# Performance work log

Measured on AMD Instinct MI355X. Metric: run time of the kernel, lower is better.

The kernel has to match this reference:

```python
import jax, jax.numpy as jnp
import numpy as np

ENC_H = 512
DEC_H = 1024

def setup_inputs() -> dict:
    key = jax.random.key(0)
    k1, k2, k3, k4 = jax.random.split(key, 4)
    B, S = 32, 2048
    s = jax.random.normal(k1, (B, DEC_H), dtype=jnp.float32)
    encoder_outputs = jax.random.normal(k2, (B, S, 2 * ENC_H), dtype=jnp.float32)
    # nn.Linear weights: attn: [dec_h, 2*enc_h + dec_h], v: [1, dec_h]
    fan_in_attn = 2 * ENC_H + DEC_H
    attn_w = jax.random.uniform(k3, (DEC_H, fan_in_attn), dtype=jnp.float32,
                                minval=-1.0, maxval=1.0) / np.sqrt(fan_in_attn)
    v_w = jax.random.uniform(k4, (1, DEC_H), dtype=jnp.float32,
                             minval=-1.0, maxval=1.0) / np.sqrt(DEC_H)
    return {"s": s, "encoder_outputs": encoder_outputs, "attn_w": attn_w, "v_w": v_w}

def reference(s, encoder_outputs, attn_w, v_w):
    # Split attn weight to avoid materializing the repeated/concatenated tensor:
    # cat([s_rep, enc], -1) @ W^T == s @ Ws^T (broadcast over S) + enc @ We^T
    W_s = attn_w[:, :DEC_H]            # [dec_h, dec_h] acts on s
    W_e = attn_w[:, DEC_H:]            # [dec_h, 2*enc_h] acts on encoder_outputs
    proj_s = jnp.einsum('bd,hd->bh', s, W_s)                   # [B, dec_h]
    proj_e = jnp.einsum('bse,he->bsh', encoder_outputs, W_e)   # [B, S, dec_h]
    energy = jnp.tanh(proj_s[:, None, :] + proj_e)             # [B, S, dec_h]
    scores = jnp.einsum('bsh,oh->bs', energy, v_w)             # [B, S]
    return jax.nn.softmax(scores, axis=1)
```

## Files before the change

kernel.cpp:

```cpp
#include <hip/hip_runtime.h>
#include <hip/hip_bf16.h>

#define KDIM 1024
#define HDIM 1024
#define BM   64

typedef __attribute__((ext_vector_type(8))) short bf16x8_t;
typedef __attribute__((ext_vector_type(16))) float f32x16_t;
typedef __attribute__((ext_vector_type(4))) float f32x4_t;
typedef __attribute__((ext_vector_type(4))) unsigned int u32x4_t;
typedef __attribute__((ext_vector_type(2))) unsigned int u32x2_t;

__device__ __forceinline__ unsigned int pack2bf(float a, float b) {
    union { float f; unsigned int u; } ua, ub;
    ua.f = a; ub.f = b;
    unsigned int ra = (ua.u + 0x7fffu + ((ua.u >> 16) & 1u)) >> 16;
    unsigned int rb = (ub.u + 0x7fffu + ((ub.u >> 16) & 1u)) >> 16;
    return ra | (rb << 16);
}

__global__ void cvt_we_k(const float* __restrict__ attn_w, unsigned short* __restrict__ we_t) {
    const int h = blockIdx.x;
    const int t = threadIdx.x;
    const f32x4_t v = *(const f32x4_t*)(attn_w + (size_t)h * 2048 + 1024 + (size_t)t * 4);
    u32x2_t o;
    o[0] = pack2bf(v[0], v[1]);
    o[1] = pack2bf(v[2], v[3]);
    const int ks  = t >> 2;
    const int e15 = (t & 3) * 4;
    *(u32x2_t*)&we_t[(size_t)ks * 16384 + h * 16 + e15] = o;
}

__global__ void proj_s_k(const float* __restrict__ s, const float* __restrict__ attn_w,
                         float* __restrict__ ps) {
    const int h = (blockIdx.x * blockDim.x + threadIdx.x) >> 6;
    const int lane = threadIdx.x & 63;
    const float* wr = attn_w + (size_t)h * 2048;
    float w[16];
#pragma unroll
    for (int i = 0; i < 16; ++i) w[i] = wr[lane + 64 * i];
    for (int b = 0; b < 32; ++b) {
        const float* sr = s + (size_t)b * 1024;
        float a = 0.f;
#pragma unroll
        for (int i = 0; i < 16; ++i) a = fmaf(w[i], sr[lane + 64 * i], a);
#pragma unroll
        for (int off = 32; off >= 1; off >>= 1) a += __shfl_xor(a, off, 64);
        if (lane == 0) ps[b * 1024 + h] = a;
    }
}

__launch_bounds__(512, 2)
__global__ void fused_main_k(const float* __restrict__ enc,
                             const unsigned short* __restrict__ we_t,
                             const float* __restrict__ ps,
                             const float* __restrict__ vw,
                             float* __restrict__ scores) {
    __shared__ unsigned short lds_a[4 * 64 * 128];

    const int t = threadIdx.x;
    const int m_base = blockIdx.x * BM;
    const int bidx = blockIdx.x >> 5;

    const int lane = t & 63;
    const int wid  = t >> 6;
    const int l31  = lane & 31;
    const int h5   = lane >> 5;
    const int hb   = wid * 128;

    const int srow = t >> 4;
    const int sc8  = t & 15;

    auto stage_load = [&](int kc, f32x4_t* r) {
#pragma unroll
        for (int i = 0; i < 2; ++i) {
            const int row = i * 32 + srow;
            const float* p = enc + (size_t)(m_base + row) * KDIM + kc * 128 + sc8 * 8;
            r[2 * i]     = __builtin_nontemporal_load((const f32x4_t*)p);
            r[2 * i + 1] = __builtin_nontemporal_load((const f32x4_t*)(p + 4));
        }
    };
    auto stage_write = [&](int kc, const f32x4_t* r) {
        const int slot = kc & 3;
#pragma unroll
        for (int i = 0; i < 2; ++i) {
            const int row = i * 32 + srow;
            u32x4_t p;
            p[0] = pack2bf(r[2 * i][0], r[2 * i][1]);
            p[1] = pack2bf(r[2 * i][2], r[2 * i][3]);
            p[2] = pack2bf(r[2 * i + 1][0], r[2 * i + 1][1]);
            p[3] = pack2bf(r[2 * i + 1][2], r[2 * i + 1][3]);
            *(u32x4_t*)&lds_a[slot * 8192 + row * 128 + ((sc8 ^ (row & 7)) << 3)] = p;
        }
    };

    const unsigned short* btile = we_t + (size_t)(hb + l31) * 16 + h5 * 8;

    f32x16_t acc[2][4];
#pragma unroll
    for (int m = 0; m < 2; ++m)
#pragma unroll
        for (int nf = 0; nf < 4; ++nf)
#pragma unroll
            for (int r = 0; r < 16; ++r) acc[m][nf][r] = 0.f;

    {
        f32x4_t r0[4], r1[4];
        stage_load(0, r0);
        stage_load(1, r1);
        stage_write(0, r0);
        stage_write(1, r1);
    }
    __syncthreads();

    const int xr = h5 ^ (l31 & 7);
    const int a0base = l31 * 128;
    const int a1base = (32 + l31) * 128;

    for (int kc = 0; kc < 8; ++kc) {
        f32x4_t rs[4];
        if (kc < 6) stage_load(kc + 2, rs);

        const unsigned short* slotp = lds_a + (kc & 3) * 8192;
        const unsigned short* bk = btile + (size_t)(kc * 8) * 16384;
#pragma unroll
        for (int ksl = 0; ksl < 8; ++ksl) {
            const int coff = ((ksl * 2) ^ xr) << 3;
            const bf16x8_t a0 = *(const bf16x8_t*)&slotp[a0base + coff];
            const bf16x8_t a1 = *(const bf16x8_t*)&slotp[a1base + coff];
            const unsigned short* bp = bk + (size_t)ksl * 16384;
            bf16x8_t bfr[4];
#pragma unroll
            for (int nf = 0; nf < 4; ++nf)
                bfr[nf] = *(const bf16x8_t*)(bp + nf * 512);
#pragma unroll
            for (int nf = 0; nf < 4; ++nf) {
                acc[0][nf] = __builtin_amdgcn_mfma_f32_32x32x16_bf16(a0, bfr[nf], acc[0][nf], 0, 0, 0);
                acc[1][nf] = __builtin_amdgcn_mfma_f32_32x32x16_bf16(a1, bfr[nf], acc[1][nf], 0, 0, 0);
            }
        }
        if (kc < 6) stage_write(kc + 2, rs);
        __syncthreads();
    }

    float sc2[2][16];
#pragma unroll
    for (int m = 0; m < 2; ++m)
#pragma unroll
        for (int r = 0; r < 16; ++r) sc2[m][r] = 0.f;

#pragma unroll
    for (int nf = 0; nf < 4; ++nf) {
        const int h = hb + nf * 32 + l31;
        const float pv = ps[bidx * 1024 + h];
        const float vv = vw[h];
#pragma unroll
        for (int m = 0; m < 2; ++m)
#pragma unroll
            for (int r = 0; r < 16; ++r) {
                const float x = acc[m][nf][r] + pv;
                const float e = __expf(2.0f * x);
                const float th = 1.0f - __fdividef(2.0f, e + 1.0f);
                sc2[m][r] = fmaf(vv, th, sc2[m][r]);
            }
    }

#pragma unroll
    for (int off = 1; off < 32; off <<= 1)
#pragma unroll
        for (int m = 0; m < 2; ++m)
#pragma unroll
            for (int r = 0; r < 16; ++r)
                sc2[m][r] += __shfl_xor(sc2[m][r], off, 64);

    __syncthreads();
    float* slds = (float*)lds_a;
    if (l31 == 0) {
#pragma unroll
        for (int m = 0; m < 2; ++m)
#pragma unroll
            for (int r = 0; r < 16; ++r) {
                const int row = m * 32 + (r & 3) + 8 * (r >> 2) + 4 * h5;
                slds[wid * 64 + row] = sc2[m][r];
            }
    }
    __syncthreads();
    if (t < 64) {
        float v = 0.f;
#pragma unroll
        for (int w = 0; w < 8; ++w) v += slds[w * 64 + t];
        scores[m_base + t] = v;
    }
}

__global__ void softmax_k(const float* __restrict__ sc, float* __restrict__ out) {
    const int b = blockIdx.x;
    const int t = threadIdx.x;
    const int lane = t & 63;
    const int w = t >> 6;
    const float* row = sc + (size_t)b * 2048;
    float x[8];
#pragma unroll
    for (int i = 0; i < 8; ++i) x[i] = row[i * 256 + t];
    float m = x[0];
#pragma unroll
    for (int i = 1; i < 8; ++i) m = fmaxf(m, x[i]);
#pragma unroll
    for (int off = 32; off >= 1; off >>= 1) m = fmaxf(m, __shfl_xor(m, off, 64));
    __shared__ float sred[4];
    __shared__ float sred2[4];
    if (lane == 0) sred[w] = m;
    __syncthreads();
    m = fmaxf(fmaxf(sred[0], sred[1]), fmaxf(sred[2], sred[3]));
    float ssum = 0.f;
#pragma unroll
    for (int i = 0; i < 8; ++i) { x[i] = expf(x[i] - m); ssum += x[i]; }
#pragma unroll
    for (int off = 32; off >= 1; off >>= 1) ssum += __shfl_xor(ssum, off, 64);
    if (lane == 0) sred2[w] = ssum;
    __syncthreads();
    const float inv = 1.0f / (sred2[0] + sred2[1] + sred2[2] + sred2[3]);
#pragma unroll
    for (int i = 0; i < 8; ++i) out[(size_t)b * 2048 + i * 256 + t] = x[i] * inv;
}

extern "C" void kernel_launch(void* const* d_in, const int* in_sizes, int n_in,
                              void* d_out, int out_size, void* d_ws, size_t ws_size,
                              hipStream_t stream) {
    const float* s      = (const float*)d_in[0];
    const float* enc    = (const float*)d_in[1];
    const float* attn_w = (const float*)d_in[2];
    const float* vw     = (const float*)d_in[3];
    float* out = (float*)d_out;

    unsigned short* we = (unsigned short*)d_ws;
    float* ps     = (float*)((char*)d_ws + (2u << 20));
    float* scores = (float*)((char*)d_ws + (2u << 20) + (128u << 10));

    cvt_we_k<<<1024, 256, 0, stream>>>(attn_w, we);
    proj_s_k<<<256, 256, 0, stream>>>(s, attn_w, ps);
    fused_main_k<<<1024, 512, 0, stream>>>(enc, we, ps, vw, scores);
    softmax_k<<<32, 256, 0, stream>>>(scores, out);
}
```

Before: 235.7 us.

## Software-pipeline B fragment loads three steps ahead and swizzle block order

```diff
diff --git a/kernel.cpp b/kernel.cpp
--- a/kernel.cpp
+++ b/kernel.cpp
@@ -59,8 +59,10 @@
     __shared__ unsigned short lds_a[4 * 64 * 128];
 
     const int t = threadIdx.x;
-    const int m_base = blockIdx.x * BM;
-    const int bidx = blockIdx.x >> 5;
+    const int bid = blockIdx.x;
+    const int swz = (bid & 7) * 128 + (bid >> 3);
+    const int m_base = swz * BM;
+    const int bidx = swz >> 5;
 
     const int lane = t & 63;
     const int wid  = t >> 6;
@@ -95,6 +97,13 @@
     };
 
     const unsigned short* btile = we_t + (size_t)(hb + l31) * 16 + h5 * 8;
+    auto loadB = [&](int g, bf16x8_t* dst) {
+        const unsigned short* bp = btile + (size_t)g * 16384;
+        dst[0] = *(const bf16x8_t*)(bp);
+        dst[1] = *(const bf16x8_t*)(bp + 512);
+        dst[2] = *(const bf16x8_t*)(bp + 1024);
+        dst[3] = *(const bf16x8_t*)(bp + 1536);
+    };
 
     f32x16_t acc[2][4];
 #pragma unroll
@@ -104,6 +113,11 @@
 #pragma unroll
             for (int r = 0; r < 16; ++r) acc[m][nf][r] = 0.f;
 
+    bf16x8_t bbuf[4][4];
+
+    loadB(0, bbuf[0]);
+    loadB(1, bbuf[1]);
+    loadB(2, bbuf[2]);
     {
         f32x4_t r0[4], r1[4];
         stage_load(0, r0);
@@ -117,30 +131,29 @@
     const int a0base = l31 * 128;
     const int a1base = (32 + l31) * 128;
 
-    for (int kc = 0; kc < 8; ++kc) {
-        f32x4_t rs[4];
-        if (kc < 6) stage_load(kc + 2, rs);
+    f32x4_t rs[4];
+#pragma unroll
+    for (int g = 0; g < 64; ++g) {
+        const int kc  = g >> 3;
+        const int ksl = g & 7;
+
+        if (g + 3 < 64) loadB(g + 3, bbuf[(g + 3) & 3]);
+        if (ksl == 3 && kc < 6) stage_load(kc + 2, rs);
 
         const unsigned short* slotp = lds_a + (kc & 3) * 8192;
-        const unsigned short* bk = btile + (size_t)(kc * 8) * 16384;
-#pragma unroll
-        for (int ksl = 0; ksl < 8; ++ksl) {
-            const int coff = ((ksl * 2) ^ xr) << 3;
-            const bf16x8_t a0 = *(const bf16x8_t*)&slotp[a0base + coff];
-            const bf16x8_t a1 = *(const bf16x8_t*)&slotp[a1base + coff];
-            const unsigned short* bp = bk + (size_t)ksl * 16384;
-            bf16x8_t bfr[4];
-#pragma unroll
-            for (int nf = 0; nf < 4; ++nf)
-                bfr[nf] = *(const bf16x8_t*)(bp + nf * 512);
-#pragma unroll
-            for (int nf = 0; nf < 4; ++nf) {
-                acc[0][nf] = __builtin_amdgcn_mfma_f32_32x32x16_bf16(a0, bfr[nf], acc[0][nf], 0, 0, 0);
-                acc[1][nf] = __builtin_amdgcn_mfma_f32_32x32x16_bf16(a1, bfr[nf], acc[1][nf], 0, 0, 0);
-            }
-        }
-        if (kc < 6) stage_write(kc + 2, rs);
-        __syncthreads();
+        const int coff = ((ksl * 2) ^ xr) << 3;
+        const bf16x8_t a0 = *(const bf16x8_t*)&slotp[a0base + coff];
+        const bf16x8_t a1 = *(const bf16x8_t*)&slotp[a1base + coff];
+        const bf16x8_t* bfr = bbuf[g & 3];
+#pragma unroll
+        for (int nf = 0; nf < 4; ++nf) {
+            acc[0][nf] = __builtin_amdgcn_mfma_f32_32x32x16_bf16(a0, bfr[nf], acc[0][nf], 0, 0, 0);
+            acc[1][nf] = __builtin_amdgcn_mfma_f32_32x32x16_bf16(a1, bfr[nf], acc[1][nf], 0, 0, 0);
+        }
+        if (ksl == 7) {
+            if (kc < 6) stage_write(kc + 2, rs);
+            __syncthreads();
+        }
     }
 
     float sc2[2][16];
```

After: 223.5 us. 5.2% less time.
